# Kernel optimization log

Hardware: AMD Instinct MI355X
Metric: run time of the kernel (lower is better)

## Reference

```python
import jax, jax.numpy as jnp
import numpy as np

EPS = 1e-8
ALPHA = 1.0

def setup_inputs() -> dict:
    key = jax.random.key(0)
    k1, k2 = jax.random.split(key)
    x = jax.random.normal(k1, (1048576, 256), dtype=jnp.float32)
    weight = jax.random.normal(k2, (65, 256), dtype=jnp.float32) * 0.02  # like trunc-normal init
    return {"x": x, "weight": weight}

def reference(x, weight):
    # x: [N, D], weight: [C, D]
    logits = x @ weight.T                             # [N, C]
    xn = jnp.linalg.norm(x, axis=1, keepdims=True)    # [N, 1]
    wn = jnp.linalg.norm(weight, axis=1)[None, :]     # [1, C]
    sim = logits / jnp.maximum(xn * wn, EPS)          # cosine similarity
    prob = jnp.power(1.0 + sim / ALPHA, (ALPHA + 1.0) / 2.0)
    return jax.nn.softmax(prob, axis=1)
```

## Files before the change

### kernel.cpp

```cpp
#include <hip/hip_runtime.h>
#include <hip/hip_bf16.h>
#include <math.h>

#define NROWS 1048576
#define D 256
#define C 65
#define MT 4
#define KS 8
#define TILES_PER_WAVE 8
#define TILES_PER_BLOCK 32

typedef float f32x4  __attribute__((ext_vector_type(4)));
typedef short bf16x8 __attribute__((ext_vector_type(8)));

__device__ __forceinline__ short f2bf(float f) {
    __hip_bfloat16 h = __float2bfloat16(f);
    return *reinterpret_cast<short*>(&h);
}

__global__ void wn_kernel(const float* __restrict__ w, float* __restrict__ wn) {
    int c = blockIdx.x;
    int l = threadIdx.x;
    float s = 0.f;
    #pragma unroll
    for (int d = l; d < D; d += 64) {
        float v = w[c * D + d];
        s = fmaf(v, v, s);
    }
    #pragma unroll
    for (int off = 32; off; off >>= 1) s += __shfl_down(s, off);
    if (l == 0) wn[c] = sqrtf(s);
}

__global__ __launch_bounds__(256, 4) void scluster_mfma(
    const float* __restrict__ x, const float* __restrict__ w,
    const float* __restrict__ wn, float* __restrict__ out)
{
    __shared__ bf16x8 wfrag[MT * KS * 64];
    __shared__ float  wb64[D];
    __shared__ float  obuf[4][16 * C];

    const int tid = threadIdx.x;

    #pragma unroll 1
    for (int f = tid; f < MT * KS * 64; f += 256) {
        const int m  = f >> 9;
        const int ks = (f >> 6) & 7;
        const int l  = f & 63;
        const int c    = m * 16 + (l & 15);
        const int koff = ks * 32 + (l >> 4) * 8;
        const float inv = __builtin_amdgcn_rcpf(wn[c]);
        const f32x4 a = *reinterpret_cast<const f32x4*>(&w[c * D + koff]);
        const f32x4 b = *reinterpret_cast<const f32x4*>(&w[c * D + koff + 4]);
        bf16x8 fr;
        fr[0] = f2bf(a.x * inv); fr[1] = f2bf(a.y * inv);
        fr[2] = f2bf(a.z * inv); fr[3] = f2bf(a.w * inv);
        fr[4] = f2bf(b.x * inv); fr[5] = f2bf(b.y * inv);
        fr[6] = f2bf(b.z * inv); fr[7] = f2bf(b.w * inv);
        wfrag[f] = fr;
    }
    if (tid < 64) {
        const float inv = __builtin_amdgcn_rcpf(wn[64]);
        const f32x4 a = *reinterpret_cast<const f32x4*>(&w[64 * D + tid * 4]);
        f32x4 v; v.x = a.x * inv; v.y = a.y * inv; v.z = a.z * inv; v.w = a.w * inv;
        *reinterpret_cast<f32x4*>(&wb64[tid * 4]) = v;
    }
    __syncthreads();

    const int wv   = tid >> 6;
    const int l    = tid & 63;
    const int g    = l >> 4;
    const int jrow = l & 15;

    const int   tile0 = blockIdx.x * TILES_PER_BLOCK + wv * TILES_PER_WAVE;
    const size_t row0 = (size_t)tile0 * 16 + jrow;
    const float* __restrict__ xp0 = x + row0 * D + g * 8;
    float* const tb = obuf[wv];

    f32x4 p[8];
    #pragma unroll
    for (int k = 0; k < 4; ++k) {
        p[2 * k]     = *reinterpret_cast<const f32x4*>(xp0 + k * 32);
        p[2 * k + 1] = *reinterpret_cast<const f32x4*>(xp0 + k * 32 + 4);
    }

    #pragma unroll 1
    for (int it = 0; it < TILES_PER_WAVE; ++it) {
        const float* __restrict__ xp = xp0 + (size_t)it * 16 * D;
        const float* __restrict__ xq = xp0 + (size_t)(it + 1) * 16 * D;

        f32x4 acc[MT];
        #pragma unroll
        for (int m = 0; m < MT; ++m) acc[m] = f32x4{0.f, 0.f, 0.f, 0.f};
        float xn2 = 0.f, acc64 = 0.f;

        bf16x8 xfA[4], xfB[4];

        #pragma unroll
        for (int k = 0; k < 4; ++k) {
            const f32x4 a = p[2 * k], b = p[2 * k + 1];
            xn2 = fmaf(a.x, a.x, xn2); xn2 = fmaf(a.y, a.y, xn2);
            xn2 = fmaf(a.z, a.z, xn2); xn2 = fmaf(a.w, a.w, xn2);
            xn2 = fmaf(b.x, b.x, xn2); xn2 = fmaf(b.y, b.y, xn2);
            xn2 = fmaf(b.z, b.z, xn2); xn2 = fmaf(b.w, b.w, xn2);
            const f32x4 wa = *reinterpret_cast<const f32x4*>(&wb64[g * 8 + k * 32]);
            const f32x4 wb = *reinterpret_cast<const f32x4*>(&wb64[g * 8 + k * 32 + 4]);
            acc64 = fmaf(wa.x, a.x, acc64); acc64 = fmaf(wa.y, a.y, acc64);
            acc64 = fmaf(wa.z, a.z, acc64); acc64 = fmaf(wa.w, a.w, acc64);
            acc64 = fmaf(wb.x, b.x, acc64); acc64 = fmaf(wb.y, b.y, acc64);
            acc64 = fmaf(wb.z, b.z, acc64); acc64 = fmaf(wb.w, b.w, acc64);
            bf16x8 xf;
            xf[0] = f2bf(a.x); xf[1] = f2bf(a.y); xf[2] = f2bf(a.z); xf[3] = f2bf(a.w);
            xf[4] = f2bf(b.x); xf[5] = f2bf(b.y); xf[6] = f2bf(b.z); xf[7] = f2bf(b.w);
            xfA[k] = xf;
        }
        #pragma unroll
        for (int k = 0; k < 4; ++k) {
            p[2 * k]     = *reinterpret_cast<const f32x4*>(xp + 128 + k * 32);
            p[2 * k + 1] = *reinterpret_cast<const f32x4*>(xp + 128 + k * 32 + 4);
        }
        __builtin_amdgcn_sched_barrier(0);
        #pragma unroll
        for (int ks = 0; ks < 4; ++ks)
            #pragma unroll
            for (int m = 0; m < MT; ++m)
                acc[m] = __builtin_amdgcn_mfma_f32_16x16x32_bf16(
                    wfrag[(m * KS + ks) * 64 + l], xfA[ks], acc[m], 0, 0, 0);

        #pragma unroll
        for (int k = 0; k < 4; ++k) {
            const f32x4 a = p[2 * k], b = p[2 * k + 1];
            xn2 = fmaf(a.x, a.x, xn2); xn2 = fmaf(a.y, a.y, xn2);
            xn2 = fmaf(a.z, a.z, xn2); xn2 = fmaf(a.w, a.w, xn2);
            xn2 = fmaf(b.x, b.x, xn2); xn2 = fmaf(b.y, b.y, xn2);
            xn2 = fmaf(b.z, b.z, xn2); xn2 = fmaf(b.w, b.w, xn2);
            const f32x4 wa = *reinterpret_cast<const f32x4*>(&wb64[g * 8 + (k + 4) * 32]);
            const f32x4 wb = *reinterpret_cast<const f32x4*>(&wb64[g * 8 + (k + 4) * 32 + 4]);
            acc64 = fmaf(wa.x, a.x, acc64); acc64 = fmaf(wa.y, a.y, acc64);
            acc64 = fmaf(wa.z, a.z, acc64); acc64 = fmaf(wa.w, a.w, acc64);
            acc64 = fmaf(wb.x, b.x, acc64); acc64 = fmaf(wb.y, b.y, acc64);
            acc64 = fmaf(wb.z, b.z, acc64); acc64 = fmaf(wb.w, b.w, acc64);
            bf16x8 xf;
            xf[0] = f2bf(a.x); xf[1] = f2bf(a.y); xf[2] = f2bf(a.z); xf[3] = f2bf(a.w);
            xf[4] = f2bf(b.x); xf[5] = f2bf(b.y); xf[6] = f2bf(b.z); xf[7] = f2bf(b.w);
            xfB[k] = xf;
        }
        if (it < TILES_PER_WAVE - 1) {
            #pragma unroll
            for (int k = 0; k < 4; ++k) {
                p[2 * k]     = *reinterpret_cast<const f32x4*>(xq + k * 32);
                p[2 * k + 1] = *reinterpret_cast<const f32x4*>(xq + k * 32 + 4);
            }
        }
        __builtin_amdgcn_sched_barrier(0);
        #pragma unroll
        for (int ks = 0; ks < 4; ++ks)
            #pragma unroll
            for (int m = 0; m < MT; ++m)
                acc[m] = __builtin_amdgcn_mfma_f32_16x16x32_bf16(
                    wfrag[(m * KS + ks + 4) * 64 + l], xfB[ks], acc[m], 0, 0, 0);

        xn2   += __shfl_xor(xn2, 16);   xn2   += __shfl_xor(xn2, 32);
        acc64 += __shfl_xor(acc64, 16); acc64 += __shfl_xor(acc64, 32);
        const float rxn = __builtin_amdgcn_rcpf(sqrtf(xn2));
        const float s64 = acc64 * rxn;

        float mx = s64;
        #pragma unroll
        for (int m = 0; m < MT; ++m) {
            #pragma unroll
            for (int r = 0; r < 4; ++r) {
                const float v = acc[m][r] * rxn;
                acc[m][r] = v;
                mx = fmaxf(mx, v);
            }
        }
        mx = fmaxf(mx, __shfl_xor(mx, 16));
        mx = fmaxf(mx, __shfl_xor(mx, 32));

        const float e64 = __expf(s64 - mx);
        float sum = (g == 0) ? e64 : 0.f;
        #pragma unroll
        for (int m = 0; m < MT; ++m) {
            #pragma unroll
            for (int r = 0; r < 4; ++r) {
                const float e = __expf(acc[m][r] - mx);
                acc[m][r] = e;
                sum += e;
            }
        }
        sum += __shfl_xor(sum, 16);
        sum += __shfl_xor(sum, 32);
        const float rs = __builtin_amdgcn_rcpf(sum);

        #pragma unroll
        for (int m = 0; m < MT; ++m) {
            #pragma unroll
            for (int r = 0; r < 4; ++r)
                tb[jrow * C + m * 16 + g * 4 + r] = acc[m][r] * rs;
        }
        if (g == 0) tb[jrow * C + 64] = e64 * rs;
        asm volatile("s_waitcnt lgkmcnt(0)" ::: "memory");

        const size_t gb = (size_t)(tile0 + it) * 16 * C;
        #pragma unroll
        for (int rd = 0; rd < 4; ++rd) {
            const int idx = rd * 64 + l;
            const f32x4 v = *reinterpret_cast<const f32x4*>(&tb[idx * 4]);
            __builtin_nontemporal_store(v, reinterpret_cast<f32x4*>(&out[gb + idx * 4]));
        }
        if (l < 4) {
            const int idx = 256 + l;
            const f32x4 v = *reinterpret_cast<const f32x4*>(&tb[idx * 4]);
            __builtin_nontemporal_store(v, reinterpret_cast<f32x4*>(&out[gb + idx * 4]));
        }
    }
}

extern "C" void kernel_launch(void* const* d_in, const int* in_sizes, int n_in,
                              void* d_out, int out_size, void* d_ws, size_t ws_size,
                              hipStream_t stream) {
    const float* x = (const float*)d_in[0];
    const float* w = (const float*)d_in[1];
    float* out = (float*)d_out;
    float* wn = (float*)d_ws;

    wn_kernel<<<C, 64, 0, stream>>>(w, wn);
    scluster_mfma<<<NROWS / 16 / TILES_PER_BLOCK, 256, 0, stream>>>(x, w, wn, out);
}
```

Before: 271.8 us.

## Shrink output staging buffer, halve tiles per wave, prefetch x before weight setup

Cuts the per-wave LDS output staging buffer from 16 rows to 4 rows, writing the tile in four passes of four rows each so the block's LDS footprint shrinks and occupancy can rise. Tiles per wave and per block are halved, which doubles the grid size. The first x tile is now loaded before the weight-fragment setup so that global load overlaps the preamble. Stores switch from nontemporal to ordinary stores, and the extra passes add more LDS waits and per-pass serialization.

```diff
diff --git a/kernel.cpp b/kernel.cpp
--- a/kernel.cpp
+++ b/kernel.cpp
@@ -7,8 +7,8 @@
 #define C 65
 #define MT 4
 #define KS 8
-#define TILES_PER_WAVE 8
-#define TILES_PER_BLOCK 32
+#define TILES_PER_WAVE 4
+#define TILES_PER_BLOCK 16
 
 typedef float f32x4  __attribute__((ext_vector_type(4)));
 typedef short bf16x8 __attribute__((ext_vector_type(8)));
@@ -38,17 +38,32 @@
 {
     __shared__ bf16x8 wfrag[MT * KS * 64];
     __shared__ float  wb64[D];
-    __shared__ float  obuf[4][16 * C];
-
-    const int tid = threadIdx.x;
+    __shared__ float  obuf[4][4 * C];
+
+    const int tid  = threadIdx.x;
+    const int wv   = tid >> 6;
+    const int l    = tid & 63;
+    const int g    = l >> 4;
+    const int jrow = l & 15;
+
+    const int   tile0 = blockIdx.x * TILES_PER_BLOCK + wv * TILES_PER_WAVE;
+    const size_t row0 = (size_t)tile0 * 16 + jrow;
+    const float* __restrict__ xp0 = x + row0 * D + g * 8;
+
+    f32x4 p[8];
+    #pragma unroll
+    for (int k = 0; k < 4; ++k) {
+        p[2 * k]     = *reinterpret_cast<const f32x4*>(xp0 + k * 32);
+        p[2 * k + 1] = *reinterpret_cast<const f32x4*>(xp0 + k * 32 + 4);
+    }
 
     #pragma unroll 1
     for (int f = tid; f < MT * KS * 64; f += 256) {
         const int m  = f >> 9;
         const int ks = (f >> 6) & 7;
-        const int l  = f & 63;
-        const int c    = m * 16 + (l & 15);
-        const int koff = ks * 32 + (l >> 4) * 8;
+        const int ll = f & 63;
+        const int c    = m * 16 + (ll & 15);
+        const int koff = ks * 32 + (ll >> 4) * 8;
         const float inv = __builtin_amdgcn_rcpf(wn[c]);
         const f32x4 a = *reinterpret_cast<const f32x4*>(&w[c * D + koff]);
         const f32x4 b = *reinterpret_cast<const f32x4*>(&w[c * D + koff + 4]);
@@ -67,22 +82,7 @@
     }
     __syncthreads();
 
-    const int wv   = tid >> 6;
-    const int l    = tid & 63;
-    const int g    = l >> 4;
-    const int jrow = l & 15;
-
-    const int   tile0 = blockIdx.x * TILES_PER_BLOCK + wv * TILES_PER_WAVE;
-    const size_t row0 = (size_t)tile0 * 16 + jrow;
-    const float* __restrict__ xp0 = x + row0 * D + g * 8;
     float* const tb = obuf[wv];
-
-    f32x4 p[8];
-    #pragma unroll
-    for (int k = 0; k < 4; ++k) {
-        p[2 * k]     = *reinterpret_cast<const f32x4*>(xp0 + k * 32);
-        p[2 * k + 1] = *reinterpret_cast<const f32x4*>(xp0 + k * 32 + 4);
-    }
 
     #pragma unroll 1
     for (int it = 0; it < TILES_PER_WAVE; ++it) {
@@ -193,26 +193,28 @@
         sum += __shfl_xor(sum, 32);
         const float rs = __builtin_amdgcn_rcpf(sum);
 
-        #pragma unroll
-        for (int m = 0; m < MT; ++m) {
-            #pragma unroll
-            for (int r = 0; r < 4; ++r)
-                tb[jrow * C + m * 16 + g * 4 + r] = acc[m][r] * rs;
-        }
-        if (g == 0) tb[jrow * C + 64] = e64 * rs;
-        asm volatile("s_waitcnt lgkmcnt(0)" ::: "memory");
-
-        const size_t gb = (size_t)(tile0 + it) * 16 * C;
-        #pragma unroll
-        for (int rd = 0; rd < 4; ++rd) {
-            const int idx = rd * 64 + l;
-            const f32x4 v = *reinterpret_cast<const f32x4*>(&tb[idx * 4]);
-            __builtin_nontemporal_store(v, reinterpret_cast<f32x4*>(&out[gb + idx * 4]));
-        }
-        if (l < 4) {
-            const int idx = 256 + l;
-            const f32x4 v = *reinterpret_cast<const f32x4*>(&tb[idx * 4]);
-            __builtin_nontemporal_store(v, reinterpret_cast<f32x4*>(&out[gb + idx * 4]));
+        const size_t gbd = (size_t)(tile0 + it) * 16 * C;
+        #pragma unroll
+        for (int ps = 0; ps < 4; ++ps) {
+            asm volatile("s_waitcnt lgkmcnt(0)" ::: "memory");
+            if ((jrow >> 2) == ps) {
+                const int r0 = (jrow & 3) * C;
+                #pragma unroll
+                for (int m = 0; m < MT; ++m) {
+                    #pragma unroll
+                    for (int r = 0; r < 4; ++r)
+                        tb[r0 + m * 16 + g * 4 + r] = acc[m][r] * rs;
+                }
+                if (g == 0) tb[r0 + 64] = e64 * rs;
+            }
+            asm volatile("s_waitcnt lgkmcnt(0)" ::: "memory");
+            const size_t go = gbd + (size_t)ps * (4 * C);
+            const f32x4 v = *reinterpret_cast<const f32x4*>(&tb[l * 4]);
+            *reinterpret_cast<f32x4*>(&out[go + l * 4]) = v;
+            if (l == 0) {
+                const f32x4 v2 = *reinterpret_cast<const f32x4*>(&tb[256]);
+                *reinterpret_cast<f32x4*>(&out[go + 256]) = v2;
+            }
         }
     }
 }
```

New measurement: 677.2 us. 149% more time.
